# Optimization experiments

Measured on AMD Instinct MI355X. Metric: run time of the kernel, lower is better.

## Reference

```python
import jax, jax.numpy as jnp
import numpy as np

C = 1.0        # curvature parameter (manifold curvature -1/C)
EPS = 1e-7


def expmap0_space(v, k):
    # v: [..., ds] spatial tangent vector at the hyperboloid origin (time comp 0)
    # returns ambient point [..., ds+1] = (sqrt(k)cosh(|v|/sqrt(k)), sqrt(k)sinh(|v|/sqrt(k)) v/|v|)
    sk = jnp.sqrt(k)
    n = jnp.maximum(jnp.linalg.norm(v, axis=-1, keepdims=True), EPS)
    t = sk * jnp.cosh(n / sk)
    s = sk * jnp.sinh(n / sk) * (v / n)
    return jnp.concatenate([t, s], axis=-1)


def logmap0_space(p, k):
    # p: [..., ds+1] hyperboloid point -> spatial tangent [..., ds] at origin
    sk = jnp.sqrt(k)
    t, s = p[..., :1], p[..., 1:]
    ns = jnp.maximum(jnp.linalg.norm(s, axis=-1, keepdims=True), EPS)
    d = sk * jnp.arccosh(jnp.maximum(t / sk, 1.0 + EPS))
    return d * (s / ns)


def setup_inputs() -> dict:
    key = jax.random.key(0)
    N, DS, E = 50000, 127, 800000
    ks = jax.random.split(key, 8)
    x = jax.random.normal(ks[0], (N, DS), dtype=jnp.float32) * 0.1
    edge_src = jax.random.randint(ks[1], (E,), 0, N)
    edge_dst = jax.random.randint(ks[2], (E,), 0, N)
    edge_weight = jax.random.uniform(ks[3], (E,), dtype=jnp.float32) / 16.0  # ~1/deg norm
    sc = 1.0 / np.sqrt(DS)
    W1 = jax.random.normal(ks[4], (DS, DS), dtype=jnp.float32) * sc
    b1 = jnp.zeros((DS,), dtype=jnp.float32)
    W2 = jax.random.normal(ks[5], (DS, DS), dtype=jnp.float32) * sc
    b2 = jnp.zeros((DS,), dtype=jnp.float32)
    return {"x": x, "W1": W1, "b1": b1, "W2": W2, "b2": b2,
            "edge_src": edge_src, "edge_dst": edge_dst, "edge_weight": edge_weight}


def reference(x, W1, b1, W2, b2, edge_src, edge_dst, edge_weight):
    N = x.shape[0]
    # encode(): cat zero time column + expmap0 onto hyperboloid
    p = expmap0_space(x, C)                 # [N, ds+1]
    h = logmap0_space(p, C)                 # tangent features at origin [N, ds]
    for (W, b) in ((W1, b1), (W2, b2)):
        # hyperbolic linear in tangent space
        z = h @ W + b                       # [N, ds]
        # adjacency-based neighbor aggregation (sparse spmm via edge list)
        msg = edge_weight[:, None] * z[edge_src]          # [E, ds] irregular gather
        agg = jax.ops.segment_sum(msg, edge_dst, num_segments=N)
        # activation + skip connection, back onto the manifold between layers
        h = jax.nn.relu(agg) + h
        h = logmap0_space(expmap0_space(h, C), C)
    return expmap0_space(h, C)              # [N, ds+1] on hyperboloid
```

## Files before the change

### kernel.cpp

```cpp
#include <hip/hip_runtime.h>

#define EPS 1e-7f
#define DS 127
#define DP 128
#define NBMAX 512
#define CAP 4096
#define CH 2048
#define PADB ((DP * DP + DP + 255) / 256)

typedef short bf16x8 __attribute__((ext_vector_type(8)));
typedef float f32x4  __attribute__((ext_vector_type(4)));
typedef float f32x2  __attribute__((ext_vector_type(2)));

__device__ __forceinline__ float wave_sum(float v) {
#pragma unroll
    for (int off = 32; off > 0; off >>= 1)
        v += __shfl_xor(v, off, 64);
    return v;
}

__device__ __forceinline__ int wave_sum_i(int v) {
#pragma unroll
    for (int off = 32; off > 0; off >>= 1)
        v += __shfl_xor(v, off, 64);
    return v;
}

__device__ __forceinline__ unsigned short f2bf(float f) {
    unsigned u = __float_as_uint(f);
    unsigned r = (u + 0x7FFFu + ((u >> 16) & 1u)) >> 16;
    return (unsigned short)r;
}

__device__ __forceinline__ unsigned pack_bf2(float a, float b) {
    return (unsigned)f2bf(a) | ((unsigned)f2bf(b) << 16);
}

__device__ __forceinline__ unsigned char f2fp8(float v) {
    return (unsigned char)(__builtin_amdgcn_cvt_pk_fp8_f32(v, v, 0, false) & 0xFF);
}

__device__ __forceinline__ float logexp_scale(float n2) {
    float nrm = sqrtf(n2);
    return (nrm >= 4.472136e-4f) ? 1.0f : (4.472136e-4f / fmaxf(nrm, EPS));
}

__device__ __forceinline__ void sinhcosh(float n, float& sh, float& ch) {
    float e  = __expf(n);
    float em = __expf(-n);
    sh = 0.5f * (e - em);
    ch = 0.5f * (e + em);
}

__global__ __launch_bounds__(256) void prep_kernel(
        const float* __restrict__ x, unsigned* __restrict__ hbu, int N,
        const float* __restrict__ W1, const float* __restrict__ b1,
        unsigned short* __restrict__ Wt1, float* __restrict__ bp1,
        const float* __restrict__ W2, const float* __restrict__ b2,
        unsigned short* __restrict__ Wt2, float* __restrict__ bp2,
        int* __restrict__ gcnt) {
    int bid = blockIdx.x;
    int tid = threadIdx.x;

    if (bid == 0) {
        for (int i = tid; i < NBMAX; i += 256) gcnt[i] = 0;
        return;
    }
    bid -= 1;

    if (bid < 2 * PADB) {
        int layer = (bid >= PADB);
        int pb    = bid - layer * PADB;
        const float* W = layer ? W2 : W1;
        const float* b = layer ? b2 : b1;
        unsigned short* Wt = layer ? Wt2 : Wt1;
        float* bp = layer ? bp2 : bp1;
        int i = pb * 256 + tid;
        if (i < DP * DP) {
            int n = i >> 7, k = i & (DP - 1);
            Wt[i] = (k < DS && n < DS) ? f2bf(W[k * DS + n]) : (unsigned short)0;
        } else if (i < DP * DP + DP) {
            int j = i - DP * DP;
            bp[j] = (j < DS) ? b[j] : 0.f;
        }
        return;
    }
    bid -= 2 * PADB;

    int gw   = bid * 4 + (tid >> 6);
    int lane = tid & 63;
    if (gw >= N) return;

    const float* row = x + (size_t)gw * DS;
    float x0 = row[2 * lane];
    float x1 = (lane < 63) ? row[2 * lane + 1] : 0.f;

    float scale = logexp_scale(wave_sum(x0 * x0 + x1 * x1));
    hbu[(size_t)gw * (DP / 2) + lane] = pack_bf2(scale * x0,
                                                 (lane < 63) ? scale * x1 : 0.f);
}

#define BM 64
__global__ __launch_bounds__(256) void gemm_mfma_kernel(
        const unsigned short* __restrict__ hb,
        const unsigned short* __restrict__ Wt,
        const float* __restrict__ bp,
        unsigned char* __restrict__ z8, int N) {
    int wave = threadIdx.x >> 6;
    int lane = threadIdx.x & 63;
    int m    = lane & 15;
    int quad = lane >> 4;
    int r0   = blockIdx.x * BM + wave * 16;

    f32x4 acc[8];
#pragma unroll
    for (int t = 0; t < 8; t++) acc[t] = (f32x4){0.f, 0.f, 0.f, 0.f};

    const bf16x8* arow = (const bf16x8*)(hb + (size_t)(r0 + m) * DP);
#pragma unroll
    for (int kq = 0; kq < 4; kq++) {
        bf16x8 a = arow[kq * 4 + quad];
#pragma unroll
        for (int nt = 0; nt < 8; nt++) {
            bf16x8 bfr = ((const bf16x8*)(Wt + (size_t)(nt * 16 + m) * DP))[kq * 4 + quad];
            acc[nt] = __builtin_amdgcn_mfma_f32_16x16x32_bf16(a, bfr, acc[nt], 0, 0, 0);
        }
    }

#pragma unroll
    for (int nt = 0; nt < 8; nt++) {
        float bias = bp[nt * 16 + m];
#pragma unroll
        for (int reg = 0; reg < 4; reg++) {
            int row = r0 + quad * 4 + reg;
            if (row < N)
                z8[(size_t)row * DP + nt * 16 + m] = f2fp8(acc[nt][reg] + bias);
        }
    }
}

__global__ __launch_bounds__(256) void binA_kernel(
        const int* __restrict__ es, const int* __restrict__ ed,
        const float* __restrict__ ew,
        int* __restrict__ gcnt, unsigned* __restrict__ stg_pk,
        unsigned char* __restrict__ stg_r, int E) {
    __shared__ int  lcnt[NBMAX];
    __shared__ int  loff[NBMAX];
    __shared__ int  gbase[NBMAX];
    __shared__ unsigned       lst_pk[CH];
    __shared__ unsigned short lst_d[CH];

    int tid  = threadIdx.x;
    int lane = tid & 63;
    int base = blockIdx.x * CH;
    int cnt  = min(CH, E - base);

    for (int b = tid; b < NBMAX; b += 256) lcnt[b] = 0;
    __syncthreads();

    unsigned pk[CH / 256];
    int      rd[CH / 256];
#pragma unroll
    for (int k = 0; k < CH / 256; k++) {
        int i = base + k * 256 + tid;
        if (i < E) {
            int d = ed[i];
            rd[k] = d;
            pk[k] = ((unsigned)f2bf(ew[i]) << 16) | (unsigned)es[i];
            atomicAdd(&lcnt[d >> 7], 1);
        } else {
            rd[k] = -1;
        }
    }
    __syncthreads();

    if (tid < 64) {
        int carry = 0;
        for (int c = 0; c < NBMAX; c += 64) {
            int v = lcnt[c + lane];
            int inc = v;
#pragma unroll
            for (int off = 1; off < 64; off <<= 1) {
                int t = __shfl_up(inc, off, 64);
                if (lane >= off) inc += t;
            }
            loff[c + lane] = carry + inc - v;
            carry += __shfl(inc, 63, 64);
        }
    }
    __syncthreads();
    for (int b = tid; b < NBMAX; b += 256) lcnt[b] = 0;
    __syncthreads();

#pragma unroll
    for (int k = 0; k < CH / 256; k++) {
        if (rd[k] >= 0) {
            int b = rd[k] >> 7;
            int slot = loff[b] + atomicAdd(&lcnt[b], 1);
            lst_pk[slot] = pk[k];
            lst_d[slot]  = (unsigned short)rd[k];
        }
    }
    __syncthreads();

    for (int b = tid; b < NBMAX; b += 256) {
        int c = lcnt[b];
        gbase[b] = c ? atomicAdd(&gcnt[b], c) : 0;
    }
    __syncthreads();

    for (int s = tid; s < cnt; s += 256) {
        unsigned p = lst_pk[s];
        int d = lst_d[s];
        int b = d >> 7;
        int idx = gbase[b] + (s - loff[b]);
        if (idx >= CAP) idx = CAP - 1;
        stg_pk[(size_t)b * CAP + idx] = p;
        stg_r [(size_t)b * CAP + idx] = (unsigned char)(d & 127);
    }
}

__global__ __launch_bounds__(256) void binB_kernel(
        const unsigned* __restrict__ stg_pk, const unsigned char* __restrict__ stg_r,
        const int* __restrict__ gcnt,
        int* __restrict__ row_start, unsigned* __restrict__ epk,
        int N, int E) {
    __shared__ int rcnt[128];
    __shared__ int roff[128];
    __shared__ int sh_bb;

    int b    = blockIdx.x;
    int tid  = threadIdx.x;
    int lane = tid & 63;
    int wave = tid >> 6;
    int cnt  = min(gcnt[b], CAP);
    const unsigned*      in_pk = stg_pk + (size_t)b * CAP;
    const unsigned char* in_r  = stg_r  + (size_t)b * CAP;

    if (tid < 128) rcnt[tid] = 0;
    if (b == 0 && tid == 0) row_start[N] = E;
    __syncthreads();

    if (wave == 3) {
        int acc = 0;
        for (int c = lane; c < b; c += 64) acc += min(gcnt[c], CAP);
        acc = wave_sum_i(acc);
        if (lane == 0) sh_bb = acc;
    } else {
        for (int i = tid; i < cnt; i += 192)
            atomicAdd(&rcnt[in_r[i]], 1);
    }
    __syncthreads();
    int bb = sh_bb;

    if (tid < 64) {
        int carry = 0;
        for (int c = 0; c < 128; c += 64) {
            int v = rcnt[c + lane];
            int inc = v;
#pragma unroll
            for (int off = 1; off < 64; off <<= 1) {
                int t = __shfl_up(inc, off, 64);
                if (lane >= off) inc += t;
            }
            roff[c + lane] = carry + inc - v;
            carry += __shfl(inc, 63, 64);
        }
    }
    __syncthreads();

    if (tid < 128) {
        int row = b * 128 + tid;
        if (row < N) row_start[row] = bb + roff[tid];
        rcnt[tid] = 0;
    }
    __syncthreads();

    for (int i = tid; i < cnt; i += 256) {
        int r = in_r[i];
        int pos = atomicAdd(&rcnt[r], 1);
        epk[bb + roff[r] + pos] = in_pk[i];
    }
}

#define GATHER(K)                                                             \
    {                                                                         \
        unsigned pks[K], us[K];                                               \
        _Pragma("unroll")                                                     \
        for (int i = 0; i < K; i++) pks[i] = epk[e + i];                      \
        _Pragma("unroll")                                                     \
        for (int i = 0; i < K; i++)                                           \
            us[i] = *(const unsigned short*)(zc + (((pks[i] & 0xFFFFu) << 7) + lane2)); \
        _Pragma("unroll")                                                     \
        for (int i = 0; i < K; i++) {                                         \
            float wf = __uint_as_float(pks[i] & 0xFFFF0000u);                 \
            f32x2 zv = __builtin_amdgcn_cvt_pk_f32_fp8(us[i], false);         \
            a0 = fmaf(wf, zv.x, a0);                                          \
            a1 = fmaf(wf, zv.y, a1);                                          \
        }                                                                     \
    }

template <bool LAST>
__global__ void agg_f_tpl(const unsigned char* __restrict__ zc,
                          const unsigned* __restrict__ hbu_in,
                          const int* __restrict__ row_start,
                          const unsigned* __restrict__ epk,
                          unsigned* __restrict__ hbu_out,
                          float* __restrict__ out, int N) {
    int gw   = (int)((blockIdx.x * blockDim.x + threadIdx.x) >> 6);
    int lane = threadIdx.x & 63;
    if (gw >= N) return;
    gw = __builtin_amdgcn_readfirstlane(gw);
    int lane2 = lane << 1;

    int beg = row_start[gw], end = row_start[gw + 1];
    float a0 = 0.f, a1 = 0.f;

    int e = beg;
    for (; e + 16 <= end; e += 16) GATHER(16)
    if (e + 8 <= end) { GATHER(8) e += 8; }
    if (e + 4 <= end) { GATHER(4) e += 4; }
    if (e + 2 <= end) { GATHER(2) e += 2; }
    if (e < end)      { GATHER(1) }

    unsigned hu = hbu_in[(size_t)gw * (DP / 2) + lane];
    float x0 = __uint_as_float(hu << 16) + fmaxf(a0, 0.f);
    float x1 = (lane < 63) ? __uint_as_float(hu & 0xFFFF0000u) + fmaxf(a1, 0.f)
                           : 0.f;

    float n2 = wave_sum(x0 * x0 + x1 * x1);
    float scale = logexp_scale(n2);
    float y0 = scale * x0;
    float y1 = (lane < 63) ? scale * x1 : 0.f;

    if (!LAST) {
        hbu_out[(size_t)gw * (DP / 2) + lane] = pack_bf2(y0, y1);
    } else {
        float n2y = scale * scale * n2;
        float ny  = fmaxf(sqrtf(n2y), EPS);
        float shy, chy;
        sinhcosh(ny, shy, chy);
        float sc  = shy / ny;
        float* orow = out + (size_t)gw * DP;
        if (lane == 0) orow[0] = chy;
        orow[1 + 2 * lane] = sc * y0;
        if (lane < 63) orow[2 + 2 * lane] = sc * y1;
    }
}

extern "C" void kernel_launch(void* const* d_in, const int* in_sizes, int n_in,
                              void* d_out, int out_size, void* d_ws, size_t ws_size,
                              hipStream_t stream) {
    const float* x  = (const float*)d_in[0];
    const float* W1 = (const float*)d_in[1];
    const float* b1 = (const float*)d_in[2];
    const float* W2 = (const float*)d_in[3];
    const float* b2 = (const float*)d_in[4];
    const int*   es = (const int*)d_in[5];
    const int*   ed = (const int*)d_in[6];
    const float* ew = (const float*)d_in[7];

    const int N  = in_sizes[0] / DS;
    const int E  = in_sizes[5];
    const int NR = (N + BM - 1) / BM * BM;
    const int NB = (N + 127) >> 7;

    unsigned short* hb  = (unsigned short*)d_ws;
    unsigned char*  z8  = (unsigned char*)(hb + (size_t)NR * DP);
    unsigned short* Wt1 = (unsigned short*)(z8 + (size_t)N * DP);
    unsigned short* Wt2 = Wt1 + DP * DP;
    float* bp1          = (float*)(Wt2 + DP * DP);
    float* bp2          = bp1 + DP;
    unsigned* epk       = (unsigned*)(bp2 + DP);
    int*   row_start    = (int*)(epk + E);
    int*   gcnt         = row_start + N + 1;
    unsigned* stg_pk    = (unsigned*)(gcnt + NBMAX);
    unsigned char* stg_r = (unsigned char*)(stg_pk + (size_t)NBMAX * CAP);

    unsigned* hbu = (unsigned*)hb;

    const int fBlocks    = (N * 64 + 255) / 256;
    const int gemmBlocks = (N + BM - 1) / BM;
    const int binABlocks = (E + CH - 1) / CH;
    const int prepBlocks = 1 + 2 * PADB + fBlocks;

    prep_kernel<<<prepBlocks, 256, 0, stream>>>(x, hbu, N,
                                                W1, b1, Wt1, bp1,
                                                W2, b2, Wt2, bp2, gcnt);

    binA_kernel<<<binABlocks, 256, 0, stream>>>(es, ed, ew, gcnt, stg_pk, stg_r, E);
    binB_kernel<<<NB, 256, 0, stream>>>(stg_pk, stg_r, gcnt, row_start, epk, N, E);

    gemm_mfma_kernel<<<gemmBlocks, 256, 0, stream>>>(hb, Wt1, bp1, z8, N);
    agg_f_tpl<false><<<fBlocks, 256, 0, stream>>>(z8, hbu, row_start, epk,
                                                  hbu, nullptr, N);

    gemm_mfma_kernel<<<gemmBlocks, 256, 0, stream>>>(hb, Wt2, bp2, z8, N);
    agg_f_tpl<true><<<fBlocks, 256, 0, stream>>>(z8, hbu, row_start, epk,
                                                 nullptr, (float*)d_out, N);
}
```

Before: 222.4 us.

## Fuse edge binning with prep and GEMM launches; simplify aggregation tail

Merges the first-pass edge binning, the weight padding and the initial logexp into one launch, and the second binning pass with the first GEMM into another launch, since the two parts of each pair do not depend on each other. The counter zeroing moves to a memset. This cuts the number of kernel launches and the serialization between independent stages. The aggregation tail now uses a single masked 16-wide gather instead of a cascade of 8/4/2/1 gathers, and launch bounds are added. In exchange, the fused kernels share their resources (shared memory from binning), which may reduce occupancy for the GEMM blocks, and the masked tail does redundant loads.

```diff
diff --git a/kernel.cpp b/kernel.cpp
--- a/kernel.cpp
+++ b/kernel.cpp
@@ -52,42 +52,22 @@
     ch = 0.5f * (e + em);
 }
 
-__global__ __launch_bounds__(256) void prep_kernel(
-        const float* __restrict__ x, unsigned* __restrict__ hbu, int N,
-        const float* __restrict__ W1, const float* __restrict__ b1,
-        unsigned short* __restrict__ Wt1, float* __restrict__ bp1,
-        const float* __restrict__ W2, const float* __restrict__ b2,
-        unsigned short* __restrict__ Wt2, float* __restrict__ bp2,
-        int* __restrict__ gcnt) {
-    int bid = blockIdx.x;
-    int tid = threadIdx.x;
-
-    if (bid == 0) {
-        for (int i = tid; i < NBMAX; i += 256) gcnt[i] = 0;
-        return;
-    }
-    bid -= 1;
-
-    if (bid < 2 * PADB) {
-        int layer = (bid >= PADB);
-        int pb    = bid - layer * PADB;
-        const float* W = layer ? W2 : W1;
-        const float* b = layer ? b2 : b1;
-        unsigned short* Wt = layer ? Wt2 : Wt1;
-        float* bp = layer ? bp2 : bp1;
-        int i = pb * 256 + tid;
-        if (i < DP * DP) {
-            int n = i >> 7, k = i & (DP - 1);
-            Wt[i] = (k < DS && n < DS) ? f2bf(W[k * DS + n]) : (unsigned short)0;
-        } else if (i < DP * DP + DP) {
-            int j = i - DP * DP;
-            bp[j] = (j < DS) ? b[j] : 0.f;
-        }
-        return;
-    }
-    bid -= 2 * PADB;
-
-    int gw   = bid * 4 + (tid >> 6);
+__device__ __forceinline__ void padT_dev(int pb, int tid,
+        const float* __restrict__ W, const float* __restrict__ b,
+        unsigned short* __restrict__ Wt, float* __restrict__ bp) {
+    int i = pb * 256 + tid;
+    if (i < DP * DP) {
+        int n = i >> 7, k = i & (DP - 1);
+        Wt[i] = (k < DS && n < DS) ? f2bf(W[k * DS + n]) : (unsigned short)0;
+    } else if (i < DP * DP + DP) {
+        int j = i - DP * DP;
+        bp[j] = (j < DS) ? b[j] : 0.f;
+    }
+}
+
+__device__ __forceinline__ void f_first_dev(int fbid, int tid,
+        const float* __restrict__ x, unsigned* __restrict__ hbu, int N) {
+    int gw   = fbid * 4 + (tid >> 6);
     int lane = tid & 63;
     if (gw >= N) return;
 
@@ -100,46 +80,7 @@
                                                  (lane < 63) ? scale * x1 : 0.f);
 }
 
-#define BM 64
-__global__ __launch_bounds__(256) void gemm_mfma_kernel(
-        const unsigned short* __restrict__ hb,
-        const unsigned short* __restrict__ Wt,
-        const float* __restrict__ bp,
-        unsigned char* __restrict__ z8, int N) {
-    int wave = threadIdx.x >> 6;
-    int lane = threadIdx.x & 63;
-    int m    = lane & 15;
-    int quad = lane >> 4;
-    int r0   = blockIdx.x * BM + wave * 16;
-
-    f32x4 acc[8];
-#pragma unroll
-    for (int t = 0; t < 8; t++) acc[t] = (f32x4){0.f, 0.f, 0.f, 0.f};
-
-    const bf16x8* arow = (const bf16x8*)(hb + (size_t)(r0 + m) * DP);
-#pragma unroll
-    for (int kq = 0; kq < 4; kq++) {
-        bf16x8 a = arow[kq * 4 + quad];
-#pragma unroll
-        for (int nt = 0; nt < 8; nt++) {
-            bf16x8 bfr = ((const bf16x8*)(Wt + (size_t)(nt * 16 + m) * DP))[kq * 4 + quad];
-            acc[nt] = __builtin_amdgcn_mfma_f32_16x16x32_bf16(a, bfr, acc[nt], 0, 0, 0);
-        }
-    }
-
-#pragma unroll
-    for (int nt = 0; nt < 8; nt++) {
-        float bias = bp[nt * 16 + m];
-#pragma unroll
-        for (int reg = 0; reg < 4; reg++) {
-            int row = r0 + quad * 4 + reg;
-            if (row < N)
-                z8[(size_t)row * DP + nt * 16 + m] = f2fp8(acc[nt][reg] + bias);
-        }
-    }
-}
-
-__global__ __launch_bounds__(256) void binA_kernel(
+__device__ void binA_dev(int abid, int tid,
         const int* __restrict__ es, const int* __restrict__ ed,
         const float* __restrict__ ew,
         int* __restrict__ gcnt, unsigned* __restrict__ stg_pk,
@@ -150,9 +91,8 @@
     __shared__ unsigned       lst_pk[CH];
     __shared__ unsigned short lst_d[CH];
 
-    int tid  = threadIdx.x;
     int lane = tid & 63;
-    int base = blockIdx.x * CH;
+    int base = abid * CH;
     int cnt  = min(CH, E - base);
 
     for (int b = tid; b < NBMAX; b += 256) lcnt[b] = 0;
@@ -220,7 +160,38 @@
     }
 }
 
-__global__ __launch_bounds__(256) void binB_kernel(
+__global__ __launch_bounds__(256) void mega1(
+        const float* __restrict__ x, unsigned* __restrict__ hbu, int N,
+        const float* __restrict__ W1, const float* __restrict__ b1,
+        unsigned short* __restrict__ Wt1, float* __restrict__ bp1,
+        const float* __restrict__ W2, const float* __restrict__ b2,
+        unsigned short* __restrict__ Wt2, float* __restrict__ bp2,
+        const int* __restrict__ es, const int* __restrict__ ed,
+        const float* __restrict__ ew,
+        int* __restrict__ gcnt, unsigned* __restrict__ stg_pk,
+        unsigned char* __restrict__ stg_r, int E, int nA) {
+    int bid = blockIdx.x;
+    int tid = threadIdx.x;
+
+    if (bid < nA) {
+        binA_dev(bid, tid, es, ed, ew, gcnt, stg_pk, stg_r, E);
+        return;
+    }
+    bid -= nA;
+
+    if (bid < 2 * PADB) {
+        int layer = (bid >= PADB);
+        int pb    = bid - layer * PADB;
+        padT_dev(pb, tid, layer ? W2 : W1, layer ? b2 : b1,
+                 layer ? Wt2 : Wt1, layer ? bp2 : bp1);
+        return;
+    }
+    bid -= 2 * PADB;
+
+    f_first_dev(bid, tid, x, hbu, N);
+}
+
+__device__ void binB_dev(int b, int tid,
         const unsigned* __restrict__ stg_pk, const unsigned char* __restrict__ stg_r,
         const int* __restrict__ gcnt,
         int* __restrict__ row_start, unsigned* __restrict__ epk,
@@ -229,8 +200,6 @@
     __shared__ int roff[128];
     __shared__ int sh_bb;
 
-    int b    = blockIdx.x;
-    int tid  = threadIdx.x;
     int lane = tid & 63;
     int wave = tid >> 6;
     int cnt  = min(gcnt[b], CAP);
@@ -283,6 +252,62 @@
     }
 }
 
+#define BM 64
+__device__ void gemm_dev(int gbid, int tid,
+        const unsigned short* __restrict__ hb,
+        const unsigned short* __restrict__ Wt,
+        const float* __restrict__ bp,
+        unsigned char* __restrict__ z8, int N) {
+    int wave = tid >> 6;
+    int lane = tid & 63;
+    int m    = lane & 15;
+    int quad = lane >> 4;
+    int r0   = gbid * BM + wave * 16;
+
+    f32x4 acc[8];
+#pragma unroll
+    for (int t = 0; t < 8; t++) acc[t] = (f32x4){0.f, 0.f, 0.f, 0.f};
+
+    const bf16x8* arow = (const bf16x8*)(hb + (size_t)(r0 + m) * DP);
+#pragma unroll
+    for (int kq = 0; kq < 4; kq++) {
+        bf16x8 a = arow[kq * 4 + quad];
+#pragma unroll
+        for (int nt = 0; nt < 8; nt++) {
+            bf16x8 bfr = ((const bf16x8*)(Wt + (size_t)(nt * 16 + m) * DP))[kq * 4 + quad];
+            acc[nt] = __builtin_amdgcn_mfma_f32_16x16x32_bf16(a, bfr, acc[nt], 0, 0, 0);
+        }
+    }
+
+#pragma unroll
+    for (int nt = 0; nt < 8; nt++) {
+        float bias = bp[nt * 16 + m];
+#pragma unroll
+        for (int reg = 0; reg < 4; reg++) {
+            int row = r0 + quad * 4 + reg;
+            if (row < N)
+                z8[(size_t)row * DP + nt * 16 + m] = f2fp8(acc[nt][reg] + bias);
+        }
+    }
+}
+
+__global__ __launch_bounds__(256) void mega2(
+        const unsigned* __restrict__ stg_pk, const unsigned char* __restrict__ stg_r,
+        const int* __restrict__ gcnt,
+        int* __restrict__ row_start, unsigned* __restrict__ epk,
+        const unsigned short* __restrict__ hb,
+        const unsigned short* __restrict__ Wt,
+        const float* __restrict__ bp,
+        unsigned char* __restrict__ z8, int N, int E, int nB) {
+    int bid = blockIdx.x;
+    int tid = threadIdx.x;
+    if (bid < nB) {
+        binB_dev(bid, tid, stg_pk, stg_r, gcnt, row_start, epk, N, E);
+        return;
+    }
+    gemm_dev(bid - nB, tid, hb, Wt, bp, z8, N);
+}
+
 #define GATHER(K)                                                             \
     {                                                                         \
         unsigned pks[K], us[K];                                               \
@@ -300,8 +325,31 @@
         }                                                                     \
     }
 
+#define GATHER_TAIL(K)                                                        \
+    {                                                                         \
+        unsigned pks[K], us[K];                                               \
+        _Pragma("unroll")                                                     \
+        for (int i = 0; i < K; i++) {                                         \
+            int ii = e + i;                                                   \
+            int ic = (ii < end) ? ii : (end - 1);                             \
+            unsigned p = epk[ic];                                             \
+            pks[i] = (ii < end) ? p : 0u;                                     \
+        }                                                                     \
+        _Pragma("unroll")                                                     \
+        for (int i = 0; i < K; i++)                                           \
+            us[i] = *(const unsigned short*)(zc + (((pks[i] & 0xFFFFu) << 7) + lane2)); \
+        _Pragma("unroll")                                                     \
+        for (int i = 0; i < K; i++) {                                         \
+            float wf = __uint_as_float(pks[i] & 0xFFFF0000u);                 \
+            f32x2 zv = __builtin_amdgcn_cvt_pk_f32_fp8(us[i], false);         \
+            a0 = fmaf(wf, zv.x, a0);                                          \
+            a1 = fmaf(wf, zv.y, a1);                                          \
+        }                                                                     \
+    }
+
 template <bool LAST>
-__global__ void agg_f_tpl(const unsigned char* __restrict__ zc,
+__global__ __launch_bounds__(256) void agg_f_tpl(
+                          const unsigned char* __restrict__ zc,
                           const unsigned* __restrict__ hbu_in,
                           const int* __restrict__ row_start,
                           const unsigned* __restrict__ epk,
@@ -318,10 +366,7 @@
 
     int e = beg;
     for (; e + 16 <= end; e += 16) GATHER(16)
-    if (e + 8 <= end) { GATHER(8) e += 8; }
-    if (e + 4 <= end) { GATHER(4) e += 4; }
-    if (e + 2 <= end) { GATHER(2) e += 2; }
-    if (e < end)      { GATHER(1) }
+    if (e < end) GATHER_TAIL(16)
 
     unsigned hu = hbu_in[(size_t)gw * (DP / 2) + lane];
     float x0 = __uint_as_float(hu << 16) + fmaxf(a0, 0.f);
@@ -382,20 +427,22 @@
     const int fBlocks    = (N * 64 + 255) / 256;
     const int gemmBlocks = (N + BM - 1) / BM;
     const int binABlocks = (E + CH - 1) / CH;
-    const int prepBlocks = 1 + 2 * PADB + fBlocks;
-
-    prep_kernel<<<prepBlocks, 256, 0, stream>>>(x, hbu, N,
-                                                W1, b1, Wt1, bp1,
-                                                W2, b2, Wt2, bp2, gcnt);
-
-    binA_kernel<<<binABlocks, 256, 0, stream>>>(es, ed, ew, gcnt, stg_pk, stg_r, E);
-    binB_kernel<<<NB, 256, 0, stream>>>(stg_pk, stg_r, gcnt, row_start, epk, N, E);
-
-    gemm_mfma_kernel<<<gemmBlocks, 256, 0, stream>>>(hb, Wt1, bp1, z8, N);
+
+    hipMemsetAsync(gcnt, 0, NBMAX * sizeof(int), stream);
+
+    mega1<<<binABlocks + 2 * PADB + fBlocks, 256, 0, stream>>>(
+        x, hbu, N, W1, b1, Wt1, bp1, W2, b2, Wt2, bp2,
+        es, ed, ew, gcnt, stg_pk, stg_r, E, binABlocks);
+
+    mega2<<<NB + gemmBlocks, 256, 0, stream>>>(
+        stg_pk, stg_r, gcnt, row_start, epk, hb, Wt1, bp1, z8, N, E, NB);
+
     agg_f_tpl<false><<<fBlocks, 256, 0, stream>>>(z8, hbu, row_start, epk,
                                                   hbu, nullptr, N);
 
-    gemm_mfma_kernel<<<gemmBlocks, 256, 0, stream>>>(hb, Wt2, bp2, z8, N);
+    mega2<<<gemmBlocks, 256, 0, stream>>>(
+        stg_pk, stg_r, gcnt, row_start, epk, hb, Wt2, bp2, z8, N, E, 0);
+
     agg_f_tpl<true><<<fBlocks, 256, 0, stream>>>(z8, hbu, row_start, epk,
                                                  nullptr, (float*)d_out, N);
 }
```

After: 220.0 us. Within noise of the previous version (-1.1%).
